# Kernel optimization log

Hardware: AMD Instinct MI355X
Metric: run time of the kernel (lower is better)

The kernel has to match this reference:

```python
import jax, jax.numpy as jnp
import numpy as np

B, T, H, DH = 4, 2048, 16, 128
D = H * DH            # inner_dim = 2048
F = 4096              # mlp_inner_dim
E = 8                 # num_expert_mlp
TOP_K = 2


def setup_inputs() -> dict:
    key = jax.random.key(0)
    ks = jax.random.split(key, 5)
    s_in = 1.0 / np.sqrt(D)
    s_f = 1.0 / np.sqrt(F)
    return {
        "stm": jax.random.normal(ks[0], (B, T, H, DH), dtype=jnp.float32),
        "gate_w": jax.random.normal(ks[1], (E, D), dtype=jnp.float32) * s_in,
        "w1": jax.random.normal(ks[2], (E, F, D), dtype=jnp.float32) * s_in,
        "w2": jax.random.normal(ks[3], (E, D, F), dtype=jnp.float32) * s_f,
        "w3": jax.random.normal(ks[4], (E, F, D), dtype=jnp.float32) * s_in,
    }


def reference(stm, gate_w, w1, w2, w3):
    b, t, h, dh = stm.shape
    d = h * dh
    x = stm.reshape(b * t, d)                                   # [N, D]
    logits = x @ gate_w.T                                       # [N, E]
    top_logit, top_idx = jax.lax.top_k(logits, TOP_K)           # [N, 2]
    gw = jax.nn.softmax(top_logit.astype(jnp.float32), axis=1).astype(x.dtype)
    out = jnp.zeros_like(x)
    n_expert = w1.shape[0]
    for e in range(n_expert):
        # combine weight for expert e per token (0 if not routed)
        we = jnp.sum(jnp.where(top_idx == e, gw, jnp.zeros_like(gw)), axis=1)  # [N]
        gate = jax.nn.silu(x @ w1[e].T)                          # [N, F]
        up = x @ w3[e].T                                         # [N, F]
        y = (gate * up) @ w2[e].T                                # [N, D]
        out = out + we[:, None] * y
    return out.reshape(b, t, h, dh)
```

## Files before the change

### kernel.cpp

```cpp
#include <hip/hip_runtime.h>
#include <hip/hip_bf16.h>
#include <stdint.h>

#define N_TOK 8192
#define DIM   2048
#define FDIM  4096
#define NEXP  8
#define BM    128
#define BN    128
#define BK    32
#define MT_MAX 64
#define HROWS_CAP 17408

#define XB_OFF   0ull
#define HB_OFF   33554432ull
#define PART_OFF 176160768ull
#define META_OFF 310378496ull
#define CNT_OFF  (META_OFF)
#define EBASE_OFF (META_OFF + 64ull)
#define ELIST_OFF (META_OFF + 128ull)
#define EWTS_OFF  (ELIST_OFF + 262144ull)
#define META_END  (EWTS_OFF + 262144ull)
#define WB_OFF    310903040ull
#define W1B_OFF   (WB_OFF)
#define W3B_OFF   (WB_OFF + 134217728ull)
#define W2B_OFF   (WB_OFF + 268435456ull)
#define WS_FULL   (WB_OFF + 402653184ull)

typedef float f32x4 __attribute__((ext_vector_type(4)));
typedef short s16x8 __attribute__((ext_vector_type(8)));

__device__ __forceinline__ uint32_t pkbf(float a, float b) {
  uint32_t ua = __builtin_bit_cast(uint32_t, a) + 0x8000u;
  uint32_t ub = __builtin_bit_cast(uint32_t, b) + 0x8000u;
  return (ua >> 16) | (ub & 0xffff0000u);
}

__device__ __forceinline__ void gld16(const void* g, void* l) {
  __builtin_amdgcn_global_load_lds(
      (__attribute__((address_space(1))) void*)g,
      (__attribute__((address_space(3))) void*)l, 16, 0, 0);
}

__global__ void init_k(int* cnt) {
  if (threadIdx.x < NEXP) cnt[threadIdx.x] = 0;
}

__global__ void router_k(const float* __restrict__ x, const float* __restrict__ gw,
                         __hip_bfloat16* __restrict__ xb, int* __restrict__ cnt,
                         int* __restrict__ elist, float* __restrict__ ewts) {
  const int n = blockIdx.x;
  const int t = threadIdx.x;
  const float* xr = x + (size_t)n * DIM;
  const float4 v0 = *(const float4*)(xr + t * 8);
  const float4 v1 = *(const float4*)(xr + t * 8 + 4);
  uint4 u;
  u.x = pkbf(v0.x, v0.y); u.y = pkbf(v0.z, v0.w);
  u.z = pkbf(v1.x, v1.y); u.w = pkbf(v1.z, v1.w);
  *(uint4*)(xb + (size_t)n * DIM + t * 8) = u;

  float p[NEXP];
#pragma unroll
  for (int e = 0; e < NEXP; ++e) {
    const float* g = gw + e * DIM + t * 8;
    const float4 g0 = *(const float4*)g;
    const float4 g1 = *(const float4*)(g + 4);
    p[e] = v0.x * g0.x + v0.y * g0.y + v0.z * g0.z + v0.w * g0.w +
           v1.x * g1.x + v1.y * g1.y + v1.z * g1.z + v1.w * g1.w;
  }
#pragma unroll
  for (int off = 32; off >= 1; off >>= 1)
#pragma unroll
    for (int e = 0; e < NEXP; ++e) p[e] += __shfl_xor(p[e], off, 64);

  __shared__ float red[4][NEXP];
  const int lane = t & 63, wv = t >> 6;
  if (lane == 0) {
#pragma unroll
    for (int e = 0; e < NEXP; ++e) red[wv][e] = p[e];
  }
  __syncthreads();
  if (t == 0) {
    float l0 = -1e30f, l1 = -1e30f;
    int e0 = 0, e1 = 0;
#pragma unroll
    for (int e = 0; e < NEXP; ++e) {
      float v = red[0][e] + red[1][e] + red[2][e] + red[3][e];
      if (v > l0) { l1 = l0; e1 = e0; l0 = v; e0 = e; }
      else if (v > l1) { l1 = v; e1 = e; }
    }
    const float ed = expf(l1 - l0);
    const float inv = 1.f / (1.f + ed);
    const float w0 = inv, w1v = ed * inv;
    int s0 = atomicAdd(cnt + e0, 1);
    elist[e0 * N_TOK + s0] = n;
    ewts[e0 * N_TOK + s0] = w0;
    int s1 = atomicAdd(cnt + e1, 1);
    elist[e1 * N_TOK + s1] = (int)((uint32_t)n | 0x80000000u);
    ewts[e1 * N_TOK + s1] = w1v;
  }
}

__global__ void scan_k(const int* __restrict__ cnt, int* __restrict__ ebase) {
  if (threadIdx.x == 0 && blockIdx.x == 0) {
    int b = 0;
    for (int e = 0; e < NEXP; ++e) { ebase[e] = b; b += (cnt[e] + BM - 1) & ~(BM - 1); }
  }
}

__global__ void convert_k(const float* __restrict__ src, __hip_bfloat16* __restrict__ dst,
                          int nchunks) {
  for (int i = blockIdx.x * blockDim.x + threadIdx.x; i < nchunks;
       i += gridDim.x * blockDim.x) {
    const float4 a = *(const float4*)(src + (size_t)i * 8);
    const float4 b = *(const float4*)(src + (size_t)i * 8 + 4);
    uint4 u;
    u.x = pkbf(a.x, a.y); u.y = pkbf(a.z, a.w);
    u.z = pkbf(b.x, b.y); u.w = pkbf(b.z, b.w);
    *(uint4*)(dst + (size_t)i * 8) = u;
  }
}

template <bool PRE>
__global__ __launch_bounds__(256, 2) void moe_up_k(
    const __hip_bfloat16* __restrict__ xb, const float* __restrict__ w1f,
    const float* __restrict__ w3f, const __hip_bfloat16* __restrict__ w1b,
    const __hip_bfloat16* __restrict__ w3b, __hip_bfloat16* __restrict__ hb,
    const int* __restrict__ cnt, const int* __restrict__ ebase,
    const int* __restrict__ elist) {
  const int e = blockIdx.z;
  const int count = cnt[e];
  const int mt = blockIdx.y;
  if (mt * BM >= count) return;
  const int nt = blockIdx.x;

  __shared__ alignas(16) __hip_bfloat16 As[2][BM * BK];
  __shared__ alignas(16) __hip_bfloat16 B1s[2][BN * BK];
  __shared__ alignas(16) __hip_bfloat16 B3s[2][BN * BK];

  const int t = threadIdx.x;
  const int lane = t & 63;
  const int wv = t >> 6;
  const int wr = wv >> 1, wc = wv & 1;
  const int r0 = t >> 2;
  const int kc = (t & 3) * 8;

  const int* lst = elist + e * N_TOK;
  int i0 = mt * BM + r0;      if (i0 >= count) i0 = 0;
  int i1 = mt * BM + r0 + 64; if (i1 >= count) i1 = 0;
  const int tok0 = lst[i0] & 0x7fffffff;
  const int tok1 = lst[i1] & 0x7fffffff;
  const __hip_bfloat16* gA0 = xb + (size_t)tok0 * DIM + kc;
  const __hip_bfloat16* gA1 = xb + (size_t)tok1 * DIM + kc;

  const size_t bO0 = ((size_t)e * FDIM + nt * BN + r0) * (size_t)DIM + kc;
  const size_t bO1 = bO0 + 64 * (size_t)DIM;

  char* AsB = (char*)As;
  char* B1sB = (char*)B1s;
  char* B3sB = (char*)B3s;
  const int ldsW = wv * 1024;

  f32x4 accG[4][4], accU[4][4];
#pragma unroll
  for (int mi = 0; mi < 4; ++mi)
#pragma unroll
    for (int ni = 0; ni < 4; ++ni) {
      accG[mi][ni] = {0.f, 0.f, 0.f, 0.f};
      accU[mi][ni] = {0.f, 0.f, 0.f, 0.f};
    }

  float4 q[8];
  auto stageA = [&](int k0, int b) {
    gld16(gA0 + k0, AsB + b * 8192 + ldsW);
    gld16(gA1 + k0, AsB + b * 8192 + 4096 + ldsW);
  };
  auto stageBpre = [&](int k0, int b) {
    gld16(w1b + bO0 + k0, B1sB + b * 8192 + ldsW);
    gld16(w1b + bO1 + k0, B1sB + b * 8192 + 4096 + ldsW);
    gld16(w3b + bO0 + k0, B3sB + b * 8192 + ldsW);
    gld16(w3b + bO1 + k0, B3sB + b * 8192 + 4096 + ldsW);
  };
  auto loadB = [&](int k0) {
    q[0] = *(const float4*)(w1f + bO0 + k0);
    q[1] = *(const float4*)(w1f + bO0 + k0 + 4);
    q[2] = *(const float4*)(w1f + bO1 + k0);
    q[3] = *(const float4*)(w1f + bO1 + k0 + 4);
    q[4] = *(const float4*)(w3f + bO0 + k0);
    q[5] = *(const float4*)(w3f + bO0 + k0 + 4);
    q[6] = *(const float4*)(w3f + bO1 + k0);
    q[7] = *(const float4*)(w3f + bO1 + k0 + 4);
  };
  auto writeB = [&](int b) {
    uint4 u;
    u.x = pkbf(q[0].x, q[0].y); u.y = pkbf(q[0].z, q[0].w);
    u.z = pkbf(q[1].x, q[1].y); u.w = pkbf(q[1].z, q[1].w);
    *(uint4*)(B1sB + b * 8192 + t * 16) = u;
    u.x = pkbf(q[2].x, q[2].y); u.y = pkbf(q[2].z, q[2].w);
    u.z = pkbf(q[3].x, q[3].y); u.w = pkbf(q[3].z, q[3].w);
    *(uint4*)(B1sB + b * 8192 + 4096 + t * 16) = u;
    u.x = pkbf(q[4].x, q[4].y); u.y = pkbf(q[4].z, q[4].w);
    u.z = pkbf(q[5].x, q[5].y); u.w = pkbf(q[5].z, q[5].w);
    *(uint4*)(B3sB + b * 8192 + t * 16) = u;
    u.x = pkbf(q[6].x, q[6].y); u.y = pkbf(q[6].z, q[6].w);
    u.z = pkbf(q[7].x, q[7].y); u.w = pkbf(q[7].z, q[7].w);
    *(uint4*)(B3sB + b * 8192 + 4096 + t * 16) = u;
  };
  auto compute = [&](int b) {
    const __hip_bfloat16* Ab = (const __hip_bfloat16*)(AsB + b * 8192);
    const __hip_bfloat16* B1b = (const __hip_bfloat16*)(B1sB + b * 8192);
    const __hip_bfloat16* B3b = (const __hip_bfloat16*)(B3sB + b * 8192);
    const int fr = lane & 15;
    const int fk = (lane >> 4) * 8;
    s16x8 af[4], b1f[4], b3f[4];
#pragma unroll
    for (int mi = 0; mi < 4; ++mi)
      af[mi] = *(const s16x8*)(Ab + (wr * 64 + mi * 16 + fr) * BK + fk);
#pragma unroll
    for (int ni = 0; ni < 4; ++ni) {
      b1f[ni] = *(const s16x8*)(B1b + (wc * 64 + ni * 16 + fr) * BK + fk);
      b3f[ni] = *(const s16x8*)(B3b + (wc * 64 + ni * 16 + fr) * BK + fk);
    }
#pragma unroll
    for (int mi = 0; mi < 4; ++mi)
#pragma unroll
      for (int ni = 0; ni < 4; ++ni) {
        accG[mi][ni] = __builtin_amdgcn_mfma_f32_16x16x32_bf16(
            af[mi], b1f[ni], accG[mi][ni], 0, 0, 0);
        accU[mi][ni] = __builtin_amdgcn_mfma_f32_16x16x32_bf16(
            af[mi], b3f[ni], accU[mi][ni], 0, 0, 0);
      }
  };

  if constexpr (PRE) {
    stageA(0, 0); stageBpre(0, 0);
  } else {
    loadB(0); stageA(0, 0); writeB(0);
  }
  __syncthreads();

  int b = 0;
  for (int kt = 0; kt < DIM / BK; ++kt) {
    const int nk = (kt + 1) * BK;
    if constexpr (PRE) {
      if (nk < DIM) { stageA(nk, b ^ 1); stageBpre(nk, b ^ 1); }
      compute(b);
    } else {
      if (nk < DIM) { loadB(nk); stageA(nk, b ^ 1); }
      compute(b);
      if (nk < DIM) writeB(b ^ 1);
    }
    __syncthreads();
    b ^= 1;
  }

  const size_t hrow0 = (size_t)ebase[e] + (size_t)(mt * BM);
  const int crow = (lane >> 4) * 4;
  const int ccol = lane & 15;
#pragma unroll
  for (int mi = 0; mi < 4; ++mi)
#pragma unroll
    for (int ni = 0; ni < 4; ++ni) {
      const int cb = nt * BN + wc * 64 + ni * 16 + ccol;
#pragma unroll
      for (int j = 0; j < 4; ++j) {
        const int r = wr * 64 + mi * 16 + crow + j;
        const float g = accG[mi][ni][j];
        const float uu = accU[mi][ni][j];
        const float h = g / (1.f + __expf(-g)) * uu;
        hb[(hrow0 + r) * (size_t)FDIM + cb] = __float2bfloat16(h);
      }
    }
}

template <bool PRE>
__global__ __launch_bounds__(256, 2) void moe_down_k(
    const __hip_bfloat16* __restrict__ hb, const float* __restrict__ w2f,
    const __hip_bfloat16* __restrict__ w2b, float* __restrict__ part,
    const int* __restrict__ cnt, const int* __restrict__ ebase,
    const int* __restrict__ elist, const float* __restrict__ ewts) {
  const int e = blockIdx.z;
  const int count = cnt[e];
  const int mt = blockIdx.y;
  if (mt * BM >= count) return;
  const int nt = blockIdx.x;

  __shared__ alignas(16) __hip_bfloat16 As[2][BM * BK];
  __shared__ alignas(16) __hip_bfloat16 Bs[2][BN * BK];

  const int t = threadIdx.x;
  const int lane = t & 63;
  const int wv = t >> 6;
  const int wr = wv >> 1, wc = wv & 1;
  const int r0 = t >> 2;
  const int kc = (t & 3) * 8;

  const size_t hrow0 = (size_t)ebase[e] + (size_t)(mt * BM);
  const __hip_bfloat16* gA0 = hb + (hrow0 + r0) * (size_t)FDIM + kc;
  const __hip_bfloat16* gA1 = gA0 + 64 * (size_t)FDIM;
  const size_t bO0 = ((size_t)e * DIM + nt * BN + r0) * (size_t)FDIM + kc;
  const size_t bO1 = bO0 + 64 * (size_t)FDIM;

  char* AsB = (char*)As;
  char* BsB = (char*)Bs;
  const int ldsW = wv * 1024;

  f32x4 acc[4][4];
#pragma unroll
  for (int mi = 0; mi < 4; ++mi)
#pragma unroll
    for (int ni = 0; ni < 4; ++ni) acc[mi][ni] = {0.f, 0.f, 0.f, 0.f};

  float4 q[4];
  auto stageA = [&](int k0, int b) {
    gld16(gA0 + k0, AsB + b * 8192 + ldsW);
    gld16(gA1 + k0, AsB + b * 8192 + 4096 + ldsW);
  };
  auto stageBpre = [&](int k0, int b) {
    gld16(w2b + bO0 + k0, BsB + b * 8192 + ldsW);
    gld16(w2b + bO1 + k0, BsB + b * 8192 + 4096 + ldsW);
  };
  auto loadB = [&](int k0) {
    q[0] = *(const float4*)(w2f + bO0 + k0);
    q[1] = *(const float4*)(w2f + bO0 + k0 + 4);
    q[2] = *(const float4*)(w2f + bO1 + k0);
    q[3] = *(const float4*)(w2f + bO1 + k0 + 4);
  };
  auto writeB = [&](int b) {
    uint4 u;
    u.x = pkbf(q[0].x, q[0].y); u.y = pkbf(q[0].z, q[0].w);
    u.z = pkbf(q[1].x, q[1].y); u.w = pkbf(q[1].z, q[1].w);
    *(uint4*)(BsB + b * 8192 + t * 16) = u;
    u.x = pkbf(q[2].x, q[2].y); u.y = pkbf(q[2].z, q[2].w);
    u.z = pkbf(q[3].x, q[3].y); u.w = pkbf(q[3].z, q[3].w);
    *(uint4*)(BsB + b * 8192 + 4096 + t * 16) = u;
  };
  auto compute = [&](int b) {
    const __hip_bfloat16* Ab = (const __hip_bfloat16*)(AsB + b * 8192);
    const __hip_bfloat16* Bb = (const __hip_bfloat16*)(BsB + b * 8192);
    const int fr = lane & 15;
    const int fk = (lane >> 4) * 8;
    s16x8 af[4], bf[4];
#pragma unroll
    for (int mi = 0; mi < 4; ++mi)
      af[mi] = *(const s16x8*)(Ab + (wr * 64 + mi * 16 + fr) * BK + fk);
#pragma unroll
    for (int ni = 0; ni < 4; ++ni)
      bf[ni] = *(const s16x8*)(Bb + (wc * 64 + ni * 16 + fr) * BK + fk);
#pragma unroll
    for (int mi = 0; mi < 4; ++mi)
#pragma unroll
      for (int ni = 0; ni < 4; ++ni)
        acc[mi][ni] = __builtin_amdgcn_mfma_f32_16x16x32_bf16(
            af[mi], bf[ni], acc[mi][ni], 0, 0, 0);
  };

  if constexpr (PRE) {
    stageA(0, 0); stageBpre(0, 0);
  } else {
    loadB(0); stageA(0, 0); writeB(0);
  }
  __syncthreads();

  int b = 0;
  for (int kt = 0; kt < FDIM / BK; ++kt) {
    const int nk = (kt + 1) * BK;
    if constexpr (PRE) {
      if (nk < FDIM) { stageA(nk, b ^ 1); stageBpre(nk, b ^ 1); }
      compute(b);
    } else {
      if (nk < FDIM) { loadB(nk); stageA(nk, b ^ 1); }
      compute(b);
      if (nk < FDIM) writeB(b ^ 1);
    }
    __syncthreads();
    b ^= 1;
  }

  const int* lst = elist + e * N_TOK;
  const float* wts = ewts + e * N_TOK;
  const int crow = (lane >> 4) * 4;
  const int ccol = lane & 15;
#pragma unroll
  for (int mi = 0; mi < 4; ++mi)
#pragma unroll
    for (int j = 0; j < 4; ++j) {
      const int i = mt * BM + wr * 64 + mi * 16 + crow + j;
      if (i < count) {
        const uint32_t info = (uint32_t)lst[i];
        const int tok = (int)(info & 0x7fffffffu);
        const int slot = (int)(info >> 31);
        const float wt = wts[i];
        float* prow = part + ((size_t)slot * N_TOK + tok) * DIM;
#pragma unroll
        for (int ni = 0; ni < 4; ++ni) {
          const int cb = nt * BN + wc * 64 + ni * 16 + ccol;
          prow[cb] = wt * acc[mi][ni][j];
        }
      }
    }
}

__global__ void combine_k(const float* __restrict__ part, float* __restrict__ out) {
  const size_t i4 = (size_t)blockIdx.x * 256 + threadIdx.x;
  const size_t idx = i4 * 4;
  const float4 a = *(const float4*)(part + idx);
  const float4 b = *(const float4*)(part + (size_t)N_TOK * DIM + idx);
  float4 o;
  o.x = a.x + b.x; o.y = a.y + b.y; o.z = a.z + b.z; o.w = a.w + b.w;
  *(float4*)(out + idx) = o;
}

extern "C" void kernel_launch(void* const* d_in, const int* in_sizes, int n_in,
                              void* d_out, int out_size, void* d_ws, size_t ws_size,
                              hipStream_t stream) {
  const float* stm = (const float*)d_in[0];
  const float* gw = (const float*)d_in[1];
  const float* w1 = (const float*)d_in[2];
  const float* w2 = (const float*)d_in[3];
  const float* w3 = (const float*)d_in[4];
  float* out = (float*)d_out;
  char* ws = (char*)d_ws;

  __hip_bfloat16* xb = (__hip_bfloat16*)(ws + XB_OFF);
  __hip_bfloat16* hb = (__hip_bfloat16*)(ws + HB_OFF);
  float* part = (float*)(ws + PART_OFF);
  int* cnt = (int*)(ws + CNT_OFF);
  int* ebase = (int*)(ws + EBASE_OFF);
  int* elist = (int*)(ws + ELIST_OFF);
  float* ewts = (float*)(ws + EWTS_OFF);
  __hip_bfloat16* w1b = (__hip_bfloat16*)(ws + W1B_OFF);
  __hip_bfloat16* w3b = (__hip_bfloat16*)(ws + W3B_OFF);
  __hip_bfloat16* w2b = (__hip_bfloat16*)(ws + W2B_OFF);

  const bool pre = (ws_size >= WS_FULL);

  init_k<<<1, 64, 0, stream>>>(cnt);
  router_k<<<N_TOK, 256, 0, stream>>>(stm, gw, xb, cnt, elist, ewts);
  scan_k<<<1, 64, 0, stream>>>(cnt, ebase);

  const dim3 gUp(FDIM / BN, MT_MAX, NEXP);
  const dim3 gDn(DIM / BN, MT_MAX, NEXP);
  const int wchunks = NEXP * FDIM * DIM / 8;

  if (pre) {
    convert_k<<<8192, 256, 0, stream>>>(w1, w1b, wchunks);
    convert_k<<<8192, 256, 0, stream>>>(w3, w3b, wchunks);
    convert_k<<<8192, 256, 0, stream>>>(w2, w2b, wchunks);
    moe_up_k<true><<<gUp, 256, 0, stream>>>(xb, w1, w3, w1b, w3b, hb, cnt, ebase, elist);
    moe_down_k<true><<<gDn, 256, 0, stream>>>(hb, w2, w2b, part, cnt, ebase, elist, ewts);
  } else {
    moe_up_k<false><<<gUp, 256, 0, stream>>>(xb, w1, w3, w1b, w3b, hb, cnt, ebase, elist);
    moe_down_k<false><<<gDn, 256, 0, stream>>>(hb, w2, w2b, part, cnt, ebase, elist, ewts);
  }

  combine_k<<<N_TOK * DIM / 1024, 256, 0, stream>>>(part, out);
}
```

Baseline: 1.634 ms.

## Replace MoE GEMMs with 256x256 tiled kernel, atomic combine, no weight preconversion

Replaces the separate up and down MoE kernels with one templated 256x256-tile GEMM using 512 threads, XOR-swizzled LDS, phased MFMA scheduling with setprio, and K=64 steps. The gate and up projections now run as two passes: the second fuses SiLU by reading back the stored bf16 gate. The down projection scatters weighted results into the output with float atomics, replacing the partial buffer and combine kernel, so a zeroing kernel is added. The bf16 weight preconversion path is dropped; fp32 weights are converted on the fly each tile. This trades more reuse per tile for extra activation passes, atomic contention, and the gate being rounded to bf16 before SiLU.

After: 1.994 ms. +22.0%, slower.

```diff
diff --git a/kernel.cpp b/kernel.cpp
--- a/kernel.cpp
+++ b/kernel.cpp
@@ -6,26 +6,16 @@
 #define DIM   2048
 #define FDIM  4096
 #define NEXP  8
-#define BM    128
-#define BN    128
-#define BK    32
-#define MT_MAX 64
-#define HROWS_CAP 17408
+#define BMN   256
+#define HROWS_CAP 18432
 
 #define XB_OFF   0ull
-#define HB_OFF   33554432ull
-#define PART_OFF 176160768ull
-#define META_OFF 310378496ull
-#define CNT_OFF  (META_OFF)
+#define GH_OFF   33554432ull
+#define META_OFF 184549376ull
+#define CNT_OFF   (META_OFF)
 #define EBASE_OFF (META_OFF + 64ull)
 #define ELIST_OFF (META_OFF + 128ull)
 #define EWTS_OFF  (ELIST_OFF + 262144ull)
-#define META_END  (EWTS_OFF + 262144ull)
-#define WB_OFF    310903040ull
-#define W1B_OFF   (WB_OFF)
-#define W3B_OFF   (WB_OFF + 134217728ull)
-#define W2B_OFF   (WB_OFF + 268435456ull)
-#define WS_FULL   (WB_OFF + 402653184ull)
 
 typedef float f32x4 __attribute__((ext_vector_type(4)));
 typedef short s16x8 __attribute__((ext_vector_type(8)));
@@ -40,6 +30,11 @@
   __builtin_amdgcn_global_load_lds(
       (__attribute__((address_space(1))) void*)g,
       (__attribute__((address_space(3))) void*)l, 16, 0, 0);
+}
+
+__global__ void zero_out_k(float* out) {
+  const size_t i = ((size_t)blockIdx.x * 256 + threadIdx.x) * 4;
+  *(float4*)(out + i) = make_float4(0.f, 0.f, 0.f, 0.f);
 }
 
 __global__ void init_k(int* cnt) {
@@ -91,324 +86,234 @@
     }
     const float ed = expf(l1 - l0);
     const float inv = 1.f / (1.f + ed);
-    const float w0 = inv, w1v = ed * inv;
     int s0 = atomicAdd(cnt + e0, 1);
     elist[e0 * N_TOK + s0] = n;
-    ewts[e0 * N_TOK + s0] = w0;
+    ewts[e0 * N_TOK + s0] = inv;
     int s1 = atomicAdd(cnt + e1, 1);
     elist[e1 * N_TOK + s1] = (int)((uint32_t)n | 0x80000000u);
-    ewts[e1 * N_TOK + s1] = w1v;
+    ewts[e1 * N_TOK + s1] = ed * inv;
   }
 }
 
 __global__ void scan_k(const int* __restrict__ cnt, int* __restrict__ ebase) {
   if (threadIdx.x == 0 && blockIdx.x == 0) {
     int b = 0;
-    for (int e = 0; e < NEXP; ++e) { ebase[e] = b; b += (cnt[e] + BM - 1) & ~(BM - 1); }
-  }
-}
-
-__global__ void convert_k(const float* __restrict__ src, __hip_bfloat16* __restrict__ dst,
-                          int nchunks) {
-  for (int i = blockIdx.x * blockDim.x + threadIdx.x; i < nchunks;
-       i += gridDim.x * blockDim.x) {
-    const float4 a = *(const float4*)(src + (size_t)i * 8);
-    const float4 b = *(const float4*)(src + (size_t)i * 8 + 4);
-    uint4 u;
-    u.x = pkbf(a.x, a.y); u.y = pkbf(a.z, a.w);
-    u.z = pkbf(b.x, b.y); u.w = pkbf(b.z, b.w);
-    *(uint4*)(dst + (size_t)i * 8) = u;
-  }
-}
-
-template <bool PRE>
-__global__ __launch_bounds__(256, 2) void moe_up_k(
-    const __hip_bfloat16* __restrict__ xb, const float* __restrict__ w1f,
-    const float* __restrict__ w3f, const __hip_bfloat16* __restrict__ w1b,
-    const __hip_bfloat16* __restrict__ w3b, __hip_bfloat16* __restrict__ hb,
+    for (int e = 0; e < NEXP; ++e) { ebase[e] = b; b += (cnt[e] + 255) & ~255; }
+  }
+}
+
+template <int KD, int MODE>
+__global__ __launch_bounds__(512, 2) void gemm256(
+    const __hip_bfloat16* __restrict__ Asrc, const float* __restrict__ Bsrc,
+    __hip_bfloat16* __restrict__ Gh, float* __restrict__ out,
     const int* __restrict__ cnt, const int* __restrict__ ebase,
-    const int* __restrict__ elist) {
+    const int* __restrict__ elist, const float* __restrict__ ewts) {
+  constexpr int NT = KD / 64;
+  constexpr int NROWS = (MODE == 2 ? DIM : FDIM);
   const int e = blockIdx.z;
   const int count = cnt[e];
   const int mt = blockIdx.y;
-  if (mt * BM >= count) return;
+  if (mt * BMN >= count) return;
   const int nt = blockIdx.x;
-
-  __shared__ alignas(16) __hip_bfloat16 As[2][BM * BK];
-  __shared__ alignas(16) __hip_bfloat16 B1s[2][BN * BK];
-  __shared__ alignas(16) __hip_bfloat16 B3s[2][BN * BK];
-
-  const int t = threadIdx.x;
-  const int lane = t & 63;
-  const int wv = t >> 6;
-  const int wr = wv >> 1, wc = wv & 1;
-  const int r0 = t >> 2;
-  const int kc = (t & 3) * 8;
-
+  const int n0 = nt * BMN;
+
+  __shared__ char lds[131072];
+
+  const int tid = threadIdx.x;
+  const int lane = tid & 63, wv = tid >> 6;
+  const int wr = wv >> 2, wc = wv & 3;
   const int* lst = elist + e * N_TOK;
-  int i0 = mt * BM + r0;      if (i0 >= count) i0 = 0;
-  int i1 = mt * BM + r0 + 64; if (i1 >= count) i1 = 0;
-  const int tok0 = lst[i0] & 0x7fffffff;
-  const int tok1 = lst[i1] & 0x7fffffff;
-  const __hip_bfloat16* gA0 = xb + (size_t)tok0 * DIM + kc;
-  const __hip_bfloat16* gA1 = xb + (size_t)tok1 * DIM + kc;
-
-  const size_t bO0 = ((size_t)e * FDIM + nt * BN + r0) * (size_t)DIM + kc;
-  const size_t bO1 = bO0 + 64 * (size_t)DIM;
-
-  char* AsB = (char*)As;
-  char* B1sB = (char*)B1s;
-  char* B3sB = (char*)B3s;
-  const int ldsW = wv * 1024;
-
-  f32x4 accG[4][4], accU[4][4];
-#pragma unroll
-  for (int mi = 0; mi < 4; ++mi)
-#pragma unroll
-    for (int ni = 0; ni < 4; ++ni) {
-      accG[mi][ni] = {0.f, 0.f, 0.f, 0.f};
-      accU[mi][ni] = {0.f, 0.f, 0.f, 0.f};
+  const size_t hrow0 = (size_t)ebase[e] + (size_t)mt * BMN;
+
+  const int g_srcA = (lane & 7) ^ (lane >> 3);
+  size_t srcAoff[2][2];
+  int ldsAoff[2][2];
+#pragma unroll
+  for (int hf = 0; hf < 2; ++hf)
+#pragma unroll
+    for (int i = 0; i < 2; ++i) {
+      const int r = hf * 128 + (2 * wv + i) * 8 + (lane >> 3);
+      size_t grow;
+      if (MODE == 2) {
+        grow = hrow0 + r;
+      } else {
+        int idx = mt * BMN + r;
+        if (idx >= count) idx = 0;
+        grow = (size_t)(lst[idx] & 0x7fffffff);
+      }
+      srcAoff[hf][i] = grow * (size_t)KD + g_srcA * 8;
+      ldsAoff[hf][i] = hf * 16384 + (2 * wv + i) * 1024;
     }
 
-  float4 q[8];
-  auto stageA = [&](int k0, int b) {
-    gld16(gA0 + k0, AsB + b * 8192 + ldsW);
-    gld16(gA1 + k0, AsB + b * 8192 + 4096 + ldsW);
-  };
-  auto stageBpre = [&](int k0, int b) {
-    gld16(w1b + bO0 + k0, B1sB + b * 8192 + ldsW);
-    gld16(w1b + bO1 + k0, B1sB + b * 8192 + 4096 + ldsW);
-    gld16(w3b + bO0 + k0, B3sB + b * 8192 + ldsW);
-    gld16(w3b + bO1 + k0, B3sB + b * 8192 + 4096 + ldsW);
-  };
-  auto loadB = [&](int k0) {
-    q[0] = *(const float4*)(w1f + bO0 + k0);
-    q[1] = *(const float4*)(w1f + bO0 + k0 + 4);
-    q[2] = *(const float4*)(w1f + bO1 + k0);
-    q[3] = *(const float4*)(w1f + bO1 + k0 + 4);
-    q[4] = *(const float4*)(w3f + bO0 + k0);
-    q[5] = *(const float4*)(w3f + bO0 + k0 + 4);
-    q[6] = *(const float4*)(w3f + bO1 + k0);
-    q[7] = *(const float4*)(w3f + bO1 + k0 + 4);
-  };
-  auto writeB = [&](int b) {
-    uint4 u;
-    u.x = pkbf(q[0].x, q[0].y); u.y = pkbf(q[0].z, q[0].w);
-    u.z = pkbf(q[1].x, q[1].y); u.w = pkbf(q[1].z, q[1].w);
-    *(uint4*)(B1sB + b * 8192 + t * 16) = u;
-    u.x = pkbf(q[2].x, q[2].y); u.y = pkbf(q[2].z, q[2].w);
-    u.z = pkbf(q[3].x, q[3].y); u.w = pkbf(q[3].z, q[3].w);
-    *(uint4*)(B1sB + b * 8192 + 4096 + t * 16) = u;
-    u.x = pkbf(q[4].x, q[4].y); u.y = pkbf(q[4].z, q[4].w);
-    u.z = pkbf(q[5].x, q[5].y); u.w = pkbf(q[5].z, q[5].w);
-    *(uint4*)(B3sB + b * 8192 + t * 16) = u;
-    u.x = pkbf(q[6].x, q[6].y); u.y = pkbf(q[6].z, q[6].w);
-    u.z = pkbf(q[7].x, q[7].y); u.w = pkbf(q[7].z, q[7].w);
-    *(uint4*)(B3sB + b * 8192 + 4096 + t * 16) = u;
-  };
-  auto compute = [&](int b) {
-    const __hip_bfloat16* Ab = (const __hip_bfloat16*)(AsB + b * 8192);
-    const __hip_bfloat16* B1b = (const __hip_bfloat16*)(B1sB + b * 8192);
-    const __hip_bfloat16* B3b = (const __hip_bfloat16*)(B3sB + b * 8192);
-    const int fr = lane & 15;
-    const int fk = (lane >> 4) * 8;
-    s16x8 af[4], b1f[4], b3f[4];
-#pragma unroll
-    for (int mi = 0; mi < 4; ++mi)
-      af[mi] = *(const s16x8*)(Ab + (wr * 64 + mi * 16 + fr) * BK + fk);
-#pragma unroll
-    for (int ni = 0; ni < 4; ++ni) {
-      b1f[ni] = *(const s16x8*)(B1b + (wc * 64 + ni * 16 + fr) * BK + fk);
-      b3f[ni] = *(const s16x8*)(B3b + (wc * 64 + ni * 16 + fr) * BK + fk);
+  const int bg = tid & 7, br = tid >> 3;
+  const int bxor = (bg ^ (br & 7)) << 4;
+  const float* srcB[2][2];
+  int ldsBoff[2][2];
+#pragma unroll
+  for (int hf = 0; hf < 2; ++hf)
+#pragma unroll
+    for (int wh = 0; wh < 2; ++wh) {
+      const int rr = hf * 128 + br + wh * 64;
+      srcB[hf][wh] = Bsrc + ((size_t)e * NROWS + n0 + rr) * (size_t)KD + bg * 8;
+      ldsBoff[hf][wh] = 65536 + hf * 16384 + (br + wh * 64) * 128 + bxor;
     }
-#pragma unroll
-    for (int mi = 0; mi < 4; ++mi)
-#pragma unroll
-      for (int ni = 0; ni < 4; ++ni) {
-        accG[mi][ni] = __builtin_amdgcn_mfma_f32_16x16x32_bf16(
-            af[mi], b1f[ni], accG[mi][ni], 0, 0, 0);
-        accU[mi][ni] = __builtin_amdgcn_mfma_f32_16x16x32_bf16(
-            af[mi], b3f[ni], accU[mi][ni], 0, 0, 0);
-      }
-  };
-
-  if constexpr (PRE) {
-    stageA(0, 0); stageBpre(0, 0);
+
+  int frag_off[2];
+#pragma unroll
+  for (int h = 0; h < 2; ++h)
+    frag_off[h] = (lane & 15) * 128 + (((h * 4 + (lane >> 4)) ^ (lane & 7)) << 4);
+  const int ardb = wr * 16384;
+  const int brdb = 65536 + (wc >> 1) * 16384 + (wc & 1) * 8192;
+
+  f32x4 acc[8][4];
+#pragma unroll
+  for (int m = 0; m < 8; ++m)
+#pragma unroll
+    for (int n = 0; n < 4; ++n) acc[m][n] = {0.f, 0.f, 0.f, 0.f};
+  s16x8 Bfr[4][2], Afr[2][2];
+  float4 ql[2][2][2];
+
+  auto stageA = [&](int t, int nb) {
+#pragma unroll
+    for (int hf = 0; hf < 2; ++hf)
+#pragma unroll
+      for (int i = 0; i < 2; ++i)
+        gld16(Asrc + srcAoff[hf][i] + t * 64, lds + nb * 32768 + ldsAoff[hf][i]);
+  };
+  auto loadB = [&](int t) {
+#pragma unroll
+    for (int hf = 0; hf < 2; ++hf)
+#pragma unroll
+      for (int wh = 0; wh < 2; ++wh) {
+        ql[hf][wh][0] = *(const float4*)(srcB[hf][wh] + t * 64);
+        ql[hf][wh][1] = *(const float4*)(srcB[hf][wh] + t * 64 + 4);
+      }
+  };
+  auto writeB = [&](int nb) {
+#pragma unroll
+    for (int hf = 0; hf < 2; ++hf)
+#pragma unroll
+      for (int wh = 0; wh < 2; ++wh) {
+        uint4 u;
+        u.x = pkbf(ql[hf][wh][0].x, ql[hf][wh][0].y);
+        u.y = pkbf(ql[hf][wh][0].z, ql[hf][wh][0].w);
+        u.z = pkbf(ql[hf][wh][1].x, ql[hf][wh][1].y);
+        u.w = pkbf(ql[hf][wh][1].z, ql[hf][wh][1].w);
+        *(uint4*)(lds + nb * 32768 + ldsBoff[hf][wh]) = u;
+      }
+  };
+  auto rdB = [&](int nb) {
+#pragma unroll
+    for (int n = 0; n < 4; ++n)
+#pragma unroll
+      for (int h = 0; h < 2; ++h)
+        Bfr[n][h] = *(const s16x8*)(lds + nb * 32768 + brdb + n * 2048 + frag_off[h]);
+  };
+  auto rdA = [&](int nb, int m0) {
+#pragma unroll
+    for (int s = 0; s < 2; ++s)
+#pragma unroll
+      for (int h = 0; h < 2; ++h)
+        Afr[s][h] = *(const s16x8*)(lds + nb * 32768 + ardb + (m0 + s) * 2048 + frag_off[h]);
+  };
+
+#define PH_PRE()                                            \
+  __builtin_amdgcn_sched_barrier(0);                        \
+  __builtin_amdgcn_s_barrier();                             \
+  __builtin_amdgcn_sched_barrier(0);                        \
+  asm volatile("s_waitcnt lgkmcnt(0)" ::: "memory");        \
+  __builtin_amdgcn_sched_barrier(0);                        \
+  __builtin_amdgcn_s_setprio(1);
+
+#define PH_POST()                                           \
+  __builtin_amdgcn_s_setprio(0);                            \
+  __builtin_amdgcn_sched_barrier(0);                        \
+  __builtin_amdgcn_s_barrier();                             \
+  __builtin_amdgcn_sched_barrier(0);
+
+#define MFMA16(M0)                                                        \
+  _Pragma("unroll") for (int h = 0; h < 2; ++h)                           \
+  _Pragma("unroll") for (int s = 0; s < 2; ++s)                           \
+  _Pragma("unroll") for (int n = 0; n < 4; ++n)                           \
+    acc[(M0) + s][n] = __builtin_amdgcn_mfma_f32_16x16x32_bf16(           \
+        Afr[s][h], Bfr[n][h], acc[(M0) + s][n], 0, 0, 0);
+
+  stageA(0, 0);
+  loadB(0); writeB(0);
+  loadB(1); writeB(1);
+  asm volatile("s_waitcnt vmcnt(0) lgkmcnt(0)" ::: "memory");
+  __builtin_amdgcn_sched_barrier(0);
+  __builtin_amdgcn_s_barrier();
+  __builtin_amdgcn_sched_barrier(0);
+
+  for (int t = 0; t < NT; ++t) {
+    const int nb = t & 1;
+    rdB(nb); rdA(nb, 0);
+    if (t + 1 < NT) stageA(t + 1, nb ^ 1);
+    PH_PRE(); MFMA16(0); PH_POST();
+    rdA(nb, 2);
+    if (t + 2 < NT) loadB(t + 2);
+    PH_PRE(); MFMA16(2); PH_POST();
+    rdA(nb, 4);
+    PH_PRE(); MFMA16(4); PH_POST();
+    rdA(nb, 6);
+    if (t + 2 < NT) writeB(nb);
+    PH_PRE(); MFMA16(6);
+    __builtin_amdgcn_s_setprio(0);
+    __builtin_amdgcn_sched_barrier(0);
+    asm volatile("s_waitcnt vmcnt(0) lgkmcnt(0)" ::: "memory");
+    __builtin_amdgcn_sched_barrier(0);
+    __builtin_amdgcn_s_barrier();
+    __builtin_amdgcn_sched_barrier(0);
+  }
+
+  const int erow = (lane >> 4) * 4;
+  const int ecol = lane & 15;
+  if constexpr (MODE == 0) {
+#pragma unroll
+    for (int m = 0; m < 8; ++m)
+#pragma unroll
+      for (int n = 0; n < 4; ++n) {
+        const size_t cb = n0 + wc * 64 + n * 16 + ecol;
+#pragma unroll
+        for (int j = 0; j < 4; ++j) {
+          const size_t r = hrow0 + wr * 128 + m * 16 + erow + j;
+          Gh[r * FDIM + cb] = __float2bfloat16(acc[m][n][j]);
+        }
+      }
+  } else if constexpr (MODE == 1) {
+#pragma unroll
+    for (int m = 0; m < 8; ++m)
+#pragma unroll
+      for (int n = 0; n < 4; ++n) {
+        const size_t cb = n0 + wc * 64 + n * 16 + ecol;
+#pragma unroll
+        for (int j = 0; j < 4; ++j) {
+          const size_t r = hrow0 + wr * 128 + m * 16 + erow + j;
+          const float g = __bfloat162float(Gh[r * FDIM + cb]);
+          const float hv = g / (1.f + __expf(-g)) * acc[m][n][j];
+          Gh[r * FDIM + cb] = __float2bfloat16(hv);
+        }
+      }
   } else {
-    loadB(0); stageA(0, 0); writeB(0);
-  }
-  __syncthreads();
-
-  int b = 0;
-  for (int kt = 0; kt < DIM / BK; ++kt) {
-    const int nk = (kt + 1) * BK;
-    if constexpr (PRE) {
-      if (nk < DIM) { stageA(nk, b ^ 1); stageBpre(nk, b ^ 1); }
-      compute(b);
-    } else {
-      if (nk < DIM) { loadB(nk); stageA(nk, b ^ 1); }
-      compute(b);
-      if (nk < DIM) writeB(b ^ 1);
-    }
-    __syncthreads();
-    b ^= 1;
-  }
-
-  const size_t hrow0 = (size_t)ebase[e] + (size_t)(mt * BM);
-  const int crow = (lane >> 4) * 4;
-  const int ccol = lane & 15;
-#pragma unroll
-  for (int mi = 0; mi < 4; ++mi)
-#pragma unroll
-    for (int ni = 0; ni < 4; ++ni) {
-      const int cb = nt * BN + wc * 64 + ni * 16 + ccol;
+#pragma unroll
+    for (int m = 0; m < 8; ++m)
 #pragma unroll
       for (int j = 0; j < 4; ++j) {
-        const int r = wr * 64 + mi * 16 + crow + j;
-        const float g = accG[mi][ni][j];
-        const float uu = accU[mi][ni][j];
-        const float h = g / (1.f + __expf(-g)) * uu;
-        hb[(hrow0 + r) * (size_t)FDIM + cb] = __float2bfloat16(h);
-      }
-    }
-}
-
-template <bool PRE>
-__global__ __launch_bounds__(256, 2) void moe_down_k(
-    const __hip_bfloat16* __restrict__ hb, const float* __restrict__ w2f,
-    const __hip_bfloat16* __restrict__ w2b, float* __restrict__ part,
-    const int* __restrict__ cnt, const int* __restrict__ ebase,
-    const int* __restrict__ elist, const float* __restrict__ ewts) {
-  const int e = blockIdx.z;
-  const int count = cnt[e];
-  const int mt = blockIdx.y;
-  if (mt * BM >= count) return;
-  const int nt = blockIdx.x;
-
-  __shared__ alignas(16) __hip_bfloat16 As[2][BM * BK];
-  __shared__ alignas(16) __hip_bfloat16 Bs[2][BN * BK];
-
-  const int t = threadIdx.x;
-  const int lane = t & 63;
-  const int wv = t >> 6;
-  const int wr = wv >> 1, wc = wv & 1;
-  const int r0 = t >> 2;
-  const int kc = (t & 3) * 8;
-
-  const size_t hrow0 = (size_t)ebase[e] + (size_t)(mt * BM);
-  const __hip_bfloat16* gA0 = hb + (hrow0 + r0) * (size_t)FDIM + kc;
-  const __hip_bfloat16* gA1 = gA0 + 64 * (size_t)FDIM;
-  const size_t bO0 = ((size_t)e * DIM + nt * BN + r0) * (size_t)FDIM + kc;
-  const size_t bO1 = bO0 + 64 * (size_t)FDIM;
-
-  char* AsB = (char*)As;
-  char* BsB = (char*)Bs;
-  const int ldsW = wv * 1024;
-
-  f32x4 acc[4][4];
-#pragma unroll
-  for (int mi = 0; mi < 4; ++mi)
-#pragma unroll
-    for (int ni = 0; ni < 4; ++ni) acc[mi][ni] = {0.f, 0.f, 0.f, 0.f};
-
-  float4 q[4];
-  auto stageA = [&](int k0, int b) {
-    gld16(gA0 + k0, AsB + b * 8192 + ldsW);
-    gld16(gA1 + k0, AsB + b * 8192 + 4096 + ldsW);
-  };
-  auto stageBpre = [&](int k0, int b) {
-    gld16(w2b + bO0 + k0, BsB + b * 8192 + ldsW);
-    gld16(w2b + bO1 + k0, BsB + b * 8192 + 4096 + ldsW);
-  };
-  auto loadB = [&](int k0) {
-    q[0] = *(const float4*)(w2f + bO0 + k0);
-    q[1] = *(const float4*)(w2f + bO0 + k0 + 4);
-    q[2] = *(const float4*)(w2f + bO1 + k0);
-    q[3] = *(const float4*)(w2f + bO1 + k0 + 4);
-  };
-  auto writeB = [&](int b) {
-    uint4 u;
-    u.x = pkbf(q[0].x, q[0].y); u.y = pkbf(q[0].z, q[0].w);
-    u.z = pkbf(q[1].x, q[1].y); u.w = pkbf(q[1].z, q[1].w);
-    *(uint4*)(BsB + b * 8192 + t * 16) = u;
-    u.x = pkbf(q[2].x, q[2].y); u.y = pkbf(q[2].z, q[2].w);
-    u.z = pkbf(q[3].x, q[3].y); u.w = pkbf(q[3].z, q[3].w);
-    *(uint4*)(BsB + b * 8192 + 4096 + t * 16) = u;
-  };
-  auto compute = [&](int b) {
-    const __hip_bfloat16* Ab = (const __hip_bfloat16*)(AsB + b * 8192);
-    const __hip_bfloat16* Bb = (const __hip_bfloat16*)(BsB + b * 8192);
-    const int fr = lane & 15;
-    const int fk = (lane >> 4) * 8;
-    s16x8 af[4], bf[4];
-#pragma unroll
-    for (int mi = 0; mi < 4; ++mi)
-      af[mi] = *(const s16x8*)(Ab + (wr * 64 + mi * 16 + fr) * BK + fk);
-#pragma unroll
-    for (int ni = 0; ni < 4; ++ni)
-      bf[ni] = *(const s16x8*)(Bb + (wc * 64 + ni * 16 + fr) * BK + fk);
-#pragma unroll
-    for (int mi = 0; mi < 4; ++mi)
-#pragma unroll
-      for (int ni = 0; ni < 4; ++ni)
-        acc[mi][ni] = __builtin_amdgcn_mfma_f32_16x16x32_bf16(
-            af[mi], bf[ni], acc[mi][ni], 0, 0, 0);
-  };
-
-  if constexpr (PRE) {
-    stageA(0, 0); stageBpre(0, 0);
-  } else {
-    loadB(0); stageA(0, 0); writeB(0);
-  }
-  __syncthreads();
-
-  int b = 0;
-  for (int kt = 0; kt < FDIM / BK; ++kt) {
-    const int nk = (kt + 1) * BK;
-    if constexpr (PRE) {
-      if (nk < FDIM) { stageA(nk, b ^ 1); stageBpre(nk, b ^ 1); }
-      compute(b);
-    } else {
-      if (nk < FDIM) { loadB(nk); stageA(nk, b ^ 1); }
-      compute(b);
-      if (nk < FDIM) writeB(b ^ 1);
-    }
-    __syncthreads();
-    b ^= 1;
-  }
-
-  const int* lst = elist + e * N_TOK;
-  const float* wts = ewts + e * N_TOK;
-  const int crow = (lane >> 4) * 4;
-  const int ccol = lane & 15;
-#pragma unroll
-  for (int mi = 0; mi < 4; ++mi)
-#pragma unroll
-    for (int j = 0; j < 4; ++j) {
-      const int i = mt * BM + wr * 64 + mi * 16 + crow + j;
-      if (i < count) {
-        const uint32_t info = (uint32_t)lst[i];
-        const int tok = (int)(info & 0x7fffffffu);
-        const int slot = (int)(info >> 31);
-        const float wt = wts[i];
-        float* prow = part + ((size_t)slot * N_TOK + tok) * DIM;
-#pragma unroll
-        for (int ni = 0; ni < 4; ++ni) {
-          const int cb = nt * BN + wc * 64 + ni * 16 + ccol;
-          prow[cb] = wt * acc[mi][ni][j];
+        const int i = mt * BMN + wr * 128 + m * 16 + erow + j;
+        if (i < count) {
+          const uint32_t info = (uint32_t)lst[i];
+          const int tok = (int)(info & 0x7fffffffu);
+          const float wt = ewts[e * N_TOK + i];
+          float* prow = out + (size_t)tok * DIM;
+#pragma unroll
+          for (int n = 0; n < 4; ++n) {
+            const int cb = n0 + wc * 64 + n * 16 + ecol;
+            atomicAdd(prow + cb, wt * acc[m][n][j]);
+          }
         }
       }
-    }
-}
-
-__global__ void combine_k(const float* __restrict__ part, float* __restrict__ out) {
-  const size_t i4 = (size_t)blockIdx.x * 256 + threadIdx.x;
-  const size_t idx = i4 * 4;
-  const float4 a = *(const float4*)(part + idx);
-  const float4 b = *(const float4*)(part + (size_t)N_TOK * DIM + idx);
-  float4 o;
-  o.x = a.x + b.x; o.y = a.y + b.y; o.z = a.z + b.z; o.w = a.w + b.w;
-  *(float4*)(out + idx) = o;
+  }
 }
 
 extern "C" void kernel_launch(void* const* d_in, const int* in_sizes, int n_in,
@@ -423,36 +328,21 @@
   char* ws = (char*)d_ws;
 
   __hip_bfloat16* xb = (__hip_bfloat16*)(ws + XB_OFF);
-  __hip_bfloat16* hb = (__hip_bfloat16*)(ws + HB_OFF);
-  float* part = (float*)(ws + PART_OFF);
+  __hip_bfloat16* Gh = (__hip_bfloat16*)(ws + GH_OFF);
   int* cnt = (int*)(ws + CNT_OFF);
   int* ebase = (int*)(ws + EBASE_OFF);
   int* elist = (int*)(ws + ELIST_OFF);
   float* ewts = (float*)(ws + EWTS_OFF);
-  __hip_bfloat16* w1b = (__hip_bfloat16*)(ws + W1B_OFF);
-  __hip_bfloat16* w3b = (__hip_bfloat16*)(ws + W3B_OFF);
-  __hip_bfloat16* w2b = (__hip_bfloat16*)(ws + W2B_OFF);
-
-  const bool pre = (ws_size >= WS_FULL);
-
+
+  zero_out_k<<<N_TOK * DIM / 1024, 256, 0, stream>>>(out);
   init_k<<<1, 64, 0, stream>>>(cnt);
   router_k<<<N_TOK, 256, 0, stream>>>(stm, gw, xb, cnt, elist, ewts);
   scan_k<<<1, 64, 0, stream>>>(cnt, ebase);
 
-  const dim3 gUp(FDIM / BN, MT_MAX, NEXP);
-  const dim3 gDn(DIM / BN, MT_MAX, NEXP);
-  const int wchunks = NEXP * FDIM * DIM / 8;
-
-  if (pre) {
-    convert_k<<<8192, 256, 0, stream>>>(w1, w1b, wchunks);
-    convert_k<<<8192, 256, 0, stream>>>(w3, w3b, wchunks);
-    convert_k<<<8192, 256, 0, stream>>>(w2, w2b, wchunks);
-    moe_up_k<true><<<gUp, 256, 0, stream>>>(xb, w1, w3, w1b, w3b, hb, cnt, ebase, elist);
-    moe_down_k<true><<<gDn, 256, 0, stream>>>(hb, w2, w2b, part, cnt, ebase, elist, ewts);
-  } else {
-    moe_up_k<false><<<gUp, 256, 0, stream>>>(xb, w1, w3, w1b, w3b, hb, cnt, ebase, elist);
-    moe_down_k<false><<<gDn, 256, 0, stream>>>(hb, w2, w2b, part, cnt, ebase, elist, ewts);
-  }
-
-  combine_k<<<N_TOK * DIM / 1024, 256, 0, stream>>>(part, out);
-}
+  const dim3 gUp(FDIM / BMN, N_TOK / BMN, NEXP);
+  const dim3 gDn(DIM / BMN, N_TOK / BMN, NEXP);
+
+  gemm256<DIM, 0><<<gUp, 512, 0, stream>>>(xb, w1, Gh, out, cnt, ebase, elist, ewts);
+  gemm256<DIM, 1><<<gUp, 512, 0, stream>>>(xb, w3, Gh, out, cnt, ebase, elist, ewts);
+  gemm256<FDIM, 2><<<gDn, 512, 0, stream>>>(Gh, w2, Gh, out, cnt, ebase, elist, ewts);
+}
```
